# Kernel tuning notes

Measured on AMD Instinct MI355X. Metric: run time of the kernel, lower is better.

Reference implementation:

```python
import jax, jax.numpy as jnp
import numpy as np

NODE_DIM = 512
HIDDEN = 4096
N_NODES = 4096  # must equal HIDDEN for pool Linear to typecheck (as in source)
N_EDGES = 131072


def setup_inputs() -> dict:
    key = jax.random.key(0)
    ks = jax.random.split(key, 12)
    s1 = 0.02
    x = jax.random.normal(ks[0], (N_NODES, NODE_DIM), dtype=jnp.float32)
    edge_index = jax.random.randint(ks[1], (2, N_EDGES), 0, N_NODES, dtype=jnp.int64)
    # encoder: Linear(node_dim, hidden) -> ReLU -> Linear(hidden, hidden)
    W1 = jax.random.normal(ks[2], (NODE_DIM, HIDDEN), dtype=jnp.float32) * s1
    b1 = jnp.zeros((HIDDEN,), dtype=jnp.float32)
    W2 = jax.random.normal(ks[3], (HIDDEN, HIDDEN), dtype=jnp.float32) * s1
    b2 = jnp.zeros((HIDDEN,), dtype=jnp.float32)
    # pool: Linear(hidden, hidden) -> ReLU -> Linear(hidden, 1)
    W3 = jax.random.normal(ks[4], (HIDDEN, HIDDEN), dtype=jnp.float32) * s1
    b3 = jnp.zeros((HIDDEN,), dtype=jnp.float32)
    W4 = jax.random.normal(ks[5], (HIDDEN, 1), dtype=jnp.float32) * s1
    b4 = jnp.zeros((1,), dtype=jnp.float32)
    return {"x": x, "edge_index": edge_index, "W1": W1, "b1": b1,
            "W2": W2, "b2": b2, "W3": W3, "b3": b3, "W4": W4, "b4": b4}


def reference(x, edge_index, W1, b1, W2, b2, W3, b3, W4, b4):
    # encoder MLP: [N, node_dim] -> [N, hidden]
    h = jax.nn.relu(x @ W1 + b1) @ W2 + b2
    # kernel_vector = (h @ h.T).sum(1) == h @ h.sum(0)  (avoids O(N^2) Gram)
    s = h.sum(axis=0)                 # [hidden]
    kernel_vector = h @ s             # [N]
    kv = kernel_vector[None, :]       # [1, N] with N == hidden
    pooled = jax.nn.relu(kv @ W3 + b3) @ W4 + b4   # [1, 1]
    return pooled
```

## Files before the change

### kernel.cpp

```cpp
#include <hip/hip_runtime.h>

#define NODES 4096
#define NDIM  512
#define HID   4096

typedef __attribute__((ext_vector_type(8))) short bf16x8;
typedef __attribute__((ext_vector_type(4))) float f32x4;

__device__ __forceinline__ float b2f(short v) {
  union { unsigned int u; float f; } c;
  c.u = ((unsigned int)(unsigned short)v) << 16;
  return c.f;
}
__device__ __forceinline__ short f2b(float f) {
  union { float f; unsigned int u; } c; c.f = f;
  unsigned int r = c.u + 0x7fffu + ((c.u >> 16) & 1u);
  return (short)(r >> 16);
}

__global__ __launch_bounds__(256) void k_cast_x(const float* __restrict__ x,
                                                short* __restrict__ xb) {
  int i = (blockIdx.x * 256 + threadIdx.x) * 4;
  float4 v = *(const float4*)(x + i);
  short4 o;
  o.x = f2b(v.x); o.y = f2b(v.y); o.z = f2b(v.z); o.w = f2b(v.w);
  *(short4*)(xb + i) = o;
}

__global__ __launch_bounds__(256) void k_transpose_w1(const float* __restrict__ W1,
                                                      short* __restrict__ w1t) {
  __shared__ float tile[32][33];
  int n0 = blockIdx.x * 32;
  int k0 = blockIdx.y * 32;
  int tx = threadIdx.x & 31, ty = threadIdx.x >> 5;
  #pragma unroll
  for (int j = 0; j < 4; ++j) {
    int kk = ty + j * 8;
    tile[kk][tx] = W1[(size_t)(k0 + kk) * HID + n0 + tx];
  }
  __syncthreads();
  #pragma unroll
  for (int j = 0; j < 4; ++j) {
    int nn = ty + j * 8;
    w1t[(size_t)(n0 + nn) * NDIM + k0 + tx] = f2b(tile[tx][nn]);
  }
}

__global__ __launch_bounds__(256) void k_init(const float* __restrict__ b2,
                                              const float* __restrict__ b3,
                                              float* __restrict__ a,
                                              float* __restrict__ s,
                                              float* __restrict__ u) {
  int j = blockIdx.x * 256 + threadIdx.x;
  a[j] = 0.0f;
  s[j] = (float)NODES * b2[j];
  u[j] = b3[j];
}

__global__ __launch_bounds__(256) void k_gemm1(const short* __restrict__ xb,
                                               const short* __restrict__ w1t,
                                               const float* __restrict__ b1,
                                               short* __restrict__ Aout,
                                               float* __restrict__ colsum) {
  __shared__ short As[128 * 32];
  __shared__ short Bs[128 * 32];
  __shared__ float csum[128];

  const int tid  = threadIdx.x;
  const int lane = tid & 63;
  const int w    = tid >> 6;
  const int wr   = w >> 1, wc = w & 1;
  const int brow = blockIdx.y * 128, bcol = blockIdx.x * 128;

  f32x4 acc[4][4];
  #pragma unroll
  for (int i = 0; i < 4; ++i)
    #pragma unroll
    for (int j = 0; j < 4; ++j)
      acc[i][j] = (f32x4){0.f, 0.f, 0.f, 0.f};

  if (tid < 128) csum[tid] = 0.f;

  const int fr = lane & 15;
  const int fk = (lane >> 4) * 8;

  for (int kt = 0; kt < NDIM / 32; ++kt) {
    __syncthreads();
    #pragma unroll
    for (int j = 0; j < 2; ++j) {
      int off = (j * 4 + w) * 1024 + lane * 16;
      int row = off >> 6, cb = off & 63;
      const short* ga = xb + (size_t)(brow + row) * NDIM + kt * 32 + (cb >> 1);
      __builtin_amdgcn_global_load_lds(
          (const __attribute__((address_space(1))) void*)ga,
          (__attribute__((address_space(3))) void*)((char*)As + off), 16, 0, 0);
      const short* gb = w1t + (size_t)(bcol + row) * NDIM + kt * 32 + (cb >> 1);
      __builtin_amdgcn_global_load_lds(
          (const __attribute__((address_space(1))) void*)gb,
          (__attribute__((address_space(3))) void*)((char*)Bs + off), 16, 0, 0);
    }
    __syncthreads();

    bf16x8 af[4], bfr[4];
    #pragma unroll
    for (int mi = 0; mi < 4; ++mi)
      af[mi] = *(const bf16x8*)(As + (wr * 64 + mi * 16 + fr) * 32 + fk);
    #pragma unroll
    for (int ni = 0; ni < 4; ++ni)
      bfr[ni] = *(const bf16x8*)(Bs + (wc * 64 + ni * 16 + fr) * 32 + fk);
    #pragma unroll
    for (int mi = 0; mi < 4; ++mi)
      #pragma unroll
      for (int ni = 0; ni < 4; ++ni)
        acc[mi][ni] = __builtin_amdgcn_mfma_f32_16x16x32_bf16(af[mi], bfr[ni],
                                                              acc[mi][ni], 0, 0, 0);
  }

  const int rbase = (lane >> 4) * 4;
  #pragma unroll
  for (int ni = 0; ni < 4; ++ni) {
    int lcol = wc * 64 + ni * 16 + fr;
    int col  = bcol + lcol;
    float bias = b1[col];
    float cl = 0.f;
    #pragma unroll
    for (int mi = 0; mi < 4; ++mi) {
      #pragma unroll
      for (int r = 0; r < 4; ++r) {
        float v = acc[mi][ni][r] + bias;
        v = v > 0.f ? v : 0.f;
        cl += v;
        int grow = brow + wr * 64 + mi * 16 + rbase + r;
        Aout[(size_t)grow * HID + col] = f2b(v);
      }
    }
    atomicAdd(&csum[lcol], cl);
  }
  __syncthreads();
  if (tid < 128) atomicAdd(&colsum[bcol + tid], csum[tid]);
}

__global__ __launch_bounds__(256) void k_gemv_at(const float* __restrict__ W,
                                                 const float* __restrict__ vin,
                                                 float* __restrict__ vout) {
  const int col = blockIdx.x * 1024 + threadIdx.x * 4;
  const int r0  = blockIdx.y * 64;
  float4 accv = {0.f, 0.f, 0.f, 0.f};
  const float* base = W + (size_t)r0 * HID + col;
  #pragma unroll 4
  for (int i = 0; i < 64; ++i) {
    float vi = vin[r0 + i];
    float4 wv = *(const float4*)(base + (size_t)i * HID);
    accv.x += vi * wv.x; accv.y += vi * wv.y;
    accv.z += vi * wv.z; accv.w += vi * wv.w;
  }
  atomicAdd(&vout[col + 0], accv.x);
  atomicAdd(&vout[col + 1], accv.y);
  atomicAdd(&vout[col + 2], accv.z);
  atomicAdd(&vout[col + 3], accv.w);
}

__global__ __launch_bounds__(256) void k_beta(const float* __restrict__ b2,
                                              const float* __restrict__ s,
                                              float* __restrict__ beta) {
  __shared__ float red[4];
  float p = 0.f;
  for (int j = threadIdx.x; j < HID; j += 256) p += b2[j] * s[j];
  #pragma unroll
  for (int o = 32; o > 0; o >>= 1) p += __shfl_down(p, o);
  int lane = threadIdx.x & 63, w = threadIdx.x >> 6;
  if (lane == 0) red[w] = p;
  __syncthreads();
  if (threadIdx.x == 0) beta[0] = red[0] + red[1] + red[2] + red[3];
}

__global__ __launch_bounds__(256) void k_gemv_row(const float* __restrict__ W,
                                                  const float* __restrict__ vin,
                                                  float* __restrict__ vout) {
  int w = threadIdx.x >> 6, lane = threadIdx.x & 63;
  int row = blockIdx.x * 4 + w;
  const float* base = W + (size_t)row * HID;
  float p = 0.f;
  for (int j = lane * 4; j < HID; j += 256) {
    float4 wv = *(const float4*)(base + j);
    float4 sv = *(const float4*)(vin + j);
    p += wv.x * sv.x + wv.y * sv.y + wv.z * sv.z + wv.w * sv.w;
  }
  #pragma unroll
  for (int o = 32; o > 0; o >>= 1) p += __shfl_down(p, o);
  if (lane == 0) vout[row] = p;
}

__global__ __launch_bounds__(256) void k_kv(const short* __restrict__ A,
                                            const float* __restrict__ t,
                                            const float* __restrict__ beta,
                                            float* __restrict__ kv) {
  int w = threadIdx.x >> 6, lane = threadIdx.x & 63;
  int row = blockIdx.x * 4 + w;
  const short* base = A + (size_t)row * HID;
  float p = 0.f;
  for (int j = lane * 8; j < HID; j += 512) {
    bf16x8 av = *(const bf16x8*)(base + j);
    float4 t0 = *(const float4*)(t + j);
    float4 t1 = *(const float4*)(t + j + 4);
    p += b2f(av[0]) * t0.x + b2f(av[1]) * t0.y + b2f(av[2]) * t0.z + b2f(av[3]) * t0.w
       + b2f(av[4]) * t1.x + b2f(av[5]) * t1.y + b2f(av[6]) * t1.z + b2f(av[7]) * t1.w;
  }
  #pragma unroll
  for (int o = 32; o > 0; o >>= 1) p += __shfl_down(p, o);
  if (lane == 0) kv[row] = p + beta[0];
}

__global__ __launch_bounds__(256) void k_final(const float* __restrict__ uacc,
                                               const float* __restrict__ W4,
                                               const float* __restrict__ b4,
                                               float* __restrict__ out) {
  __shared__ float red[4];
  float p = 0.f;
  for (int j = threadIdx.x; j < HID; j += 256) {
    float uv = uacc[j];
    uv = uv > 0.f ? uv : 0.f;
    p += uv * W4[j];
  }
  #pragma unroll
  for (int o = 32; o > 0; o >>= 1) p += __shfl_down(p, o);
  int lane = threadIdx.x & 63, w = threadIdx.x >> 6;
  if (lane == 0) red[w] = p;
  __syncthreads();
  if (threadIdx.x == 0) out[0] = red[0] + red[1] + red[2] + red[3] + b4[0];
}

extern "C" void kernel_launch(void* const* d_in, const int* in_sizes, int n_in,
                              void* d_out, int out_size, void* d_ws, size_t ws_size,
                              hipStream_t stream) {
  const float* x  = (const float*)d_in[0];
  const float* W1 = (const float*)d_in[2];
  const float* b1 = (const float*)d_in[3];
  const float* W2 = (const float*)d_in[4];
  const float* b2 = (const float*)d_in[5];
  const float* W3 = (const float*)d_in[6];
  const float* b3 = (const float*)d_in[7];
  const float* W4 = (const float*)d_in[8];
  const float* b4 = (const float*)d_in[9];
  float* out = (float*)d_out;

  char* ws = (char*)d_ws;
  short* Abf  = (short*)(ws);
  short* xb   = (short*)(ws + 33554432);
  short* w1t  = (short*)(ws + 37748736);
  float* aacc = (float*)(ws + 41943040);
  float* svec = (float*)(ws + 41959424);
  float* tvec = (float*)(ws + 41975808);
  float* kvv  = (float*)(ws + 41992192);
  float* uacc = (float*)(ws + 42008576);
  float* beta = (float*)(ws + 42024960);

  k_cast_x      <<<dim3(NODES * NDIM / 1024), dim3(256), 0, stream>>>(x, xb);
  k_transpose_w1<<<dim3(128, 16),             dim3(256), 0, stream>>>(W1, w1t);
  k_init        <<<dim3(16),                  dim3(256), 0, stream>>>(b2, b3, aacc, svec, uacc);
  k_gemm1       <<<dim3(32, 32),              dim3(256), 0, stream>>>(xb, w1t, b1, Abf, aacc);
  k_gemv_at     <<<dim3(4, 64),               dim3(256), 0, stream>>>(W2, aacc, svec);
  k_beta        <<<dim3(1),                   dim3(256), 0, stream>>>(b2, svec, beta);
  k_gemv_row    <<<dim3(1024),                dim3(256), 0, stream>>>(W2, svec, tvec);
  k_kv          <<<dim3(1024),                dim3(256), 0, stream>>>(Abf, tvec, beta, kvv);
  k_gemv_at     <<<dim3(4, 64),               dim3(256), 0, stream>>>(W3, kvv, uacc);
  k_final       <<<dim3(1),                   dim3(256), 0, stream>>>(uacc, W4, b4, out);
}
```

Measured before the change: 106.2 us.

## Fuse prep kernels, double-buffer GEMM1 and coalesce its output via LDS

Merges the cast, transpose and init kernels into one launch and folds the beta reduction into the row GEMV as an extra block. GEMM1 now double-buffers its LDS tiles, overlapping the next stage's global-to-LDS loads with MFMA work. Its epilogue stages the bf16 tile in swizzled LDS so the output is written as coalesced 16-byte stores. The column GEMV uses twice as many blocks with shorter row chunks, at the cost of more atomics, and some loops get unroll hints.

Result: slower. 126.2 us (+18.9%).

```diff
diff --git a/kernel.cpp b/kernel.cpp
--- a/kernel.cpp
+++ b/kernel.cpp
@@ -18,43 +18,45 @@
   return (short)(r >> 16);
 }
 
-__global__ __launch_bounds__(256) void k_cast_x(const float* __restrict__ x,
-                                                short* __restrict__ xb) {
-  int i = (blockIdx.x * 256 + threadIdx.x) * 4;
-  float4 v = *(const float4*)(x + i);
-  short4 o;
-  o.x = f2b(v.x); o.y = f2b(v.y); o.z = f2b(v.z); o.w = f2b(v.w);
-  *(short4*)(xb + i) = o;
-}
-
-__global__ __launch_bounds__(256) void k_transpose_w1(const float* __restrict__ W1,
-                                                      short* __restrict__ w1t) {
+__global__ __launch_bounds__(256) void k_prep(const float* __restrict__ x,
+                                              const float* __restrict__ W1,
+                                              const float* __restrict__ b2,
+                                              const float* __restrict__ b3,
+                                              short* __restrict__ xb,
+                                              short* __restrict__ w1t,
+                                              float* __restrict__ aacc,
+                                              float* __restrict__ svec,
+                                              float* __restrict__ uacc) {
   __shared__ float tile[32][33];
-  int n0 = blockIdx.x * 32;
-  int k0 = blockIdx.y * 32;
-  int tx = threadIdx.x & 31, ty = threadIdx.x >> 5;
-  #pragma unroll
-  for (int j = 0; j < 4; ++j) {
-    int kk = ty + j * 8;
-    tile[kk][tx] = W1[(size_t)(k0 + kk) * HID + n0 + tx];
-  }
-  __syncthreads();
-  #pragma unroll
-  for (int j = 0; j < 4; ++j) {
-    int nn = ty + j * 8;
-    w1t[(size_t)(n0 + nn) * NDIM + k0 + tx] = f2b(tile[tx][nn]);
-  }
-}
-
-__global__ __launch_bounds__(256) void k_init(const float* __restrict__ b2,
-                                              const float* __restrict__ b3,
-                                              float* __restrict__ a,
-                                              float* __restrict__ s,
-                                              float* __restrict__ u) {
-  int j = blockIdx.x * 256 + threadIdx.x;
-  a[j] = 0.0f;
-  s[j] = (float)NODES * b2[j];
-  u[j] = b3[j];
+  int b = blockIdx.x;
+  if (b < 2048) {
+    int i = (b * 256 + threadIdx.x) * 4;
+    float4 v = *(const float4*)(x + i);
+    short4 o;
+    o.x = f2b(v.x); o.y = f2b(v.y); o.z = f2b(v.z); o.w = f2b(v.w);
+    *(short4*)(xb + i) = o;
+  } else if (b < 4096) {
+    int t = b - 2048;
+    int n0 = (t & 127) * 32;
+    int k0 = (t >> 7) * 32;
+    int tx = threadIdx.x & 31, ty = threadIdx.x >> 5;
+    #pragma unroll
+    for (int j = 0; j < 4; ++j) {
+      int kk = ty + j * 8;
+      tile[kk][tx] = W1[(size_t)(k0 + kk) * HID + n0 + tx];
+    }
+    __syncthreads();
+    #pragma unroll
+    for (int j = 0; j < 4; ++j) {
+      int nn = ty + j * 8;
+      w1t[(size_t)(n0 + nn) * NDIM + k0 + tx] = f2b(tile[tx][nn]);
+    }
+  } else {
+    int j = (b - 4096) * 256 + threadIdx.x;
+    aacc[j] = 0.0f;
+    svec[j] = (float)NODES * b2[j];
+    uacc[j] = b3[j];
+  }
 }
 
 __global__ __launch_bounds__(256) void k_gemm1(const short* __restrict__ xb,
@@ -62,8 +64,7 @@
                                                const float* __restrict__ b1,
                                                short* __restrict__ Aout,
                                                float* __restrict__ colsum) {
-  __shared__ short As[128 * 32];
-  __shared__ short Bs[128 * 32];
+  __shared__ short smem[16384];
   __shared__ float csum[128];
 
   const int tid  = threadIdx.x;
@@ -84,59 +85,96 @@
   const int fr = lane & 15;
   const int fk = (lane >> 4) * 8;
 
-  for (int kt = 0; kt < NDIM / 32; ++kt) {
-    __syncthreads();
+  auto STAGE = [&](int buf, int kt) {
     #pragma unroll
     for (int j = 0; j < 2; ++j) {
       int off = (j * 4 + w) * 1024 + lane * 16;
-      int row = off >> 6, cb = off & 63;
-      const short* ga = xb + (size_t)(brow + row) * NDIM + kt * 32 + (cb >> 1);
+      int row = off >> 6, ce = (off & 63) >> 1;
+      const short* ga = xb + (size_t)(brow + row) * NDIM + kt * 32 + ce;
       __builtin_amdgcn_global_load_lds(
           (const __attribute__((address_space(1))) void*)ga,
-          (__attribute__((address_space(3))) void*)((char*)As + off), 16, 0, 0);
-      const short* gb = w1t + (size_t)(bcol + row) * NDIM + kt * 32 + (cb >> 1);
+          (__attribute__((address_space(3))) void*)((char*)smem + buf * 8192 + off),
+          16, 0, 0);
+      const short* gb = w1t + (size_t)(bcol + row) * NDIM + kt * 32 + ce;
       __builtin_amdgcn_global_load_lds(
           (const __attribute__((address_space(1))) void*)gb,
-          (__attribute__((address_space(3))) void*)((char*)Bs + off), 16, 0, 0);
+          (__attribute__((address_space(3))) void*)((char*)smem + 16384 + buf * 8192 + off),
+          16, 0, 0);
     }
-    __syncthreads();
-
+  };
+
+  STAGE(0, 0);
+  __syncthreads();
+  int cur = 0;
+  #pragma unroll 1
+  for (int kt = 0; kt < NDIM / 32 - 1; ++kt) {
+    STAGE(cur ^ 1, kt + 1);
     bf16x8 af[4], bfr[4];
+    const short* Ab = (const short*)((char*)smem + cur * 8192);
+    const short* Bb = (const short*)((char*)smem + 16384 + cur * 8192);
     #pragma unroll
     for (int mi = 0; mi < 4; ++mi)
-      af[mi] = *(const bf16x8*)(As + (wr * 64 + mi * 16 + fr) * 32 + fk);
+      af[mi] = *(const bf16x8*)(Ab + (wr * 64 + mi * 16 + fr) * 32 + fk);
     #pragma unroll
     for (int ni = 0; ni < 4; ++ni)
-      bfr[ni] = *(const bf16x8*)(Bs + (wc * 64 + ni * 16 + fr) * 32 + fk);
+      bfr[ni] = *(const bf16x8*)(Bb + (wc * 64 + ni * 16 + fr) * 32 + fk);
     #pragma unroll
     for (int mi = 0; mi < 4; ++mi)
       #pragma unroll
       for (int ni = 0; ni < 4; ++ni)
         acc[mi][ni] = __builtin_amdgcn_mfma_f32_16x16x32_bf16(af[mi], bfr[ni],
                                                               acc[mi][ni], 0, 0, 0);
-  }
+    __syncthreads();
+    cur ^= 1;
+  }
+  {
+    bf16x8 af[4], bfr[4];
+    const short* Ab = (const short*)((char*)smem + cur * 8192);
+    const short* Bb = (const short*)((char*)smem + 16384 + cur * 8192);
+    #pragma unroll
+    for (int mi = 0; mi < 4; ++mi)
+      af[mi] = *(const bf16x8*)(Ab + (wr * 64 + mi * 16 + fr) * 32 + fk);
+    #pragma unroll
+    for (int ni = 0; ni < 4; ++ni)
+      bfr[ni] = *(const bf16x8*)(Bb + (wc * 64 + ni * 16 + fr) * 32 + fk);
+    #pragma unroll
+    for (int mi = 0; mi < 4; ++mi)
+      #pragma unroll
+      for (int ni = 0; ni < 4; ++ni)
+        acc[mi][ni] = __builtin_amdgcn_mfma_f32_16x16x32_bf16(af[mi], bfr[ni],
+                                                              acc[mi][ni], 0, 0, 0);
+  }
+  __syncthreads();
 
   const int rbase = (lane >> 4) * 4;
   #pragma unroll
   for (int ni = 0; ni < 4; ++ni) {
     int lcol = wc * 64 + ni * 16 + fr;
-    int col  = bcol + lcol;
-    float bias = b1[col];
+    float bias = b1[bcol + lcol];
     float cl = 0.f;
     #pragma unroll
     for (int mi = 0; mi < 4; ++mi) {
       #pragma unroll
       for (int r = 0; r < 4; ++r) {
         float v = acc[mi][ni][r] + bias;
-        v = v > 0.f ? v : 0.f;
+        v = fmaxf(v, 0.f);
         cl += v;
-        int grow = brow + wr * 64 + mi * 16 + rbase + r;
-        Aout[(size_t)grow * HID + col] = f2b(v);
+        int lrow = wr * 64 + mi * 16 + rbase + r;
+        int boff = (lrow * 256 + lcol * 2) ^ ((lrow & 7) << 4);
+        *(short*)((char*)smem + boff) = f2b(v);
       }
     }
     atomicAdd(&csum[lcol], cl);
   }
   __syncthreads();
+  #pragma unroll
+  for (int i = 0; i < 8; ++i) {
+    int c = i * 256 + tid;
+    int lrow = c >> 4;
+    int boff = (c * 16) ^ ((lrow & 7) << 4);
+    bf16x8 vv = *(const bf16x8*)((char*)smem + boff);
+    *(bf16x8*)(Aout + (size_t)(brow + lrow) * HID + bcol + (c & 15) * 8) = vv;
+  }
   if (tid < 128) atomicAdd(&colsum[bcol + tid], csum[tid]);
 }
 
@@ -144,11 +182,11 @@
                                                  const float* __restrict__ vin,
                                                  float* __restrict__ vout) {
   const int col = blockIdx.x * 1024 + threadIdx.x * 4;
-  const int r0  = blockIdx.y * 64;
+  const int r0  = blockIdx.y * 32;
   float4 accv = {0.f, 0.f, 0.f, 0.f};
   const float* base = W + (size_t)r0 * HID + col;
-  #pragma unroll 4
-  for (int i = 0; i < 64; ++i) {
+  #pragma unroll 8
+  for (int i = 0; i < 32; ++i) {
     float vi = vin[r0 + i];
     float4 wv = *(const float4*)(base + (size_t)i * HID);
     accv.x += vi * wv.x; accv.y += vi * wv.y;
@@ -160,27 +198,28 @@
   atomicAdd(&vout[col + 3], accv.w);
 }
 
-__global__ __launch_bounds__(256) void k_beta(const float* __restrict__ b2,
-                                              const float* __restrict__ s,
-                                              float* __restrict__ beta) {
-  __shared__ float red[4];
-  float p = 0.f;
-  for (int j = threadIdx.x; j < HID; j += 256) p += b2[j] * s[j];
-  #pragma unroll
-  for (int o = 32; o > 0; o >>= 1) p += __shfl_down(p, o);
-  int lane = threadIdx.x & 63, w = threadIdx.x >> 6;
-  if (lane == 0) red[w] = p;
-  __syncthreads();
-  if (threadIdx.x == 0) beta[0] = red[0] + red[1] + red[2] + red[3];
-}
-
 __global__ __launch_bounds__(256) void k_gemv_row(const float* __restrict__ W,
                                                   const float* __restrict__ vin,
-                                                  float* __restrict__ vout) {
+                                                  const float* __restrict__ b2,
+                                                  float* __restrict__ vout,
+                                                  float* __restrict__ beta) {
+  __shared__ float red[4];
+  if (blockIdx.x == HID / 4) {
+    float p = 0.f;
+    for (int j = threadIdx.x; j < HID; j += 256) p += b2[j] * vin[j];
+    #pragma unroll
+    for (int o = 32; o > 0; o >>= 1) p += __shfl_down(p, o);
+    int lane = threadIdx.x & 63, w = threadIdx.x >> 6;
+    if (lane == 0) red[w] = p;
+    __syncthreads();
+    if (threadIdx.x == 0) beta[0] = red[0] + red[1] + red[2] + red[3];
+    return;
+  }
   int w = threadIdx.x >> 6, lane = threadIdx.x & 63;
   int row = blockIdx.x * 4 + w;
   const float* base = W + (size_t)row * HID;
   float p = 0.f;
+  #pragma unroll 4
   for (int j = lane * 4; j < HID; j += 256) {
     float4 wv = *(const float4*)(base + j);
     float4 sv = *(const float4*)(vin + j);
@@ -199,6 +238,7 @@
   int row = blockIdx.x * 4 + w;
   const short* base = A + (size_t)row * HID;
   float p = 0.f;
+  #pragma unroll
   for (int j = lane * 8; j < HID; j += 512) {
     bf16x8 av = *(const bf16x8*)(base + j);
     float4 t0 = *(const float4*)(t + j);
@@ -255,14 +295,11 @@
   float* uacc = (float*)(ws + 42008576);
   float* beta = (float*)(ws + 42024960);
 
-  k_cast_x      <<<dim3(NODES * NDIM / 1024), dim3(256), 0, stream>>>(x, xb);
-  k_transpose_w1<<<dim3(128, 16),             dim3(256), 0, stream>>>(W1, w1t);
-  k_init        <<<dim3(16),                  dim3(256), 0, stream>>>(b2, b3, aacc, svec, uacc);
-  k_gemm1       <<<dim3(32, 32),              dim3(256), 0, stream>>>(xb, w1t, b1, Abf, aacc);
-  k_gemv_at     <<<dim3(4, 64),               dim3(256), 0, stream>>>(W2, aacc, svec);
-  k_beta        <<<dim3(1),                   dim3(256), 0, stream>>>(b2, svec, beta);
-  k_gemv_row    <<<dim3(1024),                dim3(256), 0, stream>>>(W2, svec, tvec);
-  k_kv          <<<dim3(1024),                dim3(256), 0, stream>>>(Abf, tvec, beta, kvv);
-  k_gemv_at     <<<dim3(4, 64),               dim3(256), 0, stream>>>(W3, kvv, uacc);
-  k_final       <<<dim3(1),                   dim3(256), 0, stream>>>(uacc, W4, b4, out);
-}
+  k_prep    <<<dim3(4112),     dim3(256), 0, stream>>>(x, W1, b2, b3, xb, w1t, aacc, svec, uacc);
+  k_gemm1   <<<dim3(32, 32),   dim3(256), 0, stream>>>(xb, w1t, b1, Abf, aacc);
+  k_gemv_at <<<dim3(4, 128),   dim3(256), 0, stream>>>(W2, aacc, svec);
+  k_gemv_row<<<dim3(1025),     dim3(256), 0, stream>>>(W2, svec, b2, tvec, beta);
+  k_kv      <<<dim3(1024),     dim3(256), 0, stream>>>(Abf, tvec, beta, kvv);
+  k_gemv_at <<<dim3(4, 128),   dim3(256), 0, stream>>>(W3, kvv, uacc);
+  k_final   <<<dim3(1),        dim3(256), 0, stream>>>(uacc, W4, b4, out);
+}
```
